# Optimization experiments

Hardware: AMD Instinct MI355X
Metric: run time of the kernel (lower is better)

Reference implementation:

```python
import jax, jax.numpy as jnp
import numpy as np

KERNEL_SIZE = 4  # kernel_size=4, dim=1, degree-1 open B-splines (SplineConv defaults)


def spline_conv(x, edge_index, edge_attr, W, root, bias):
    """SplineConv with dim=1, kernel_size=4, degree=1, open splines, aggr='mean'.

    x: [N, F_in]; edge_index: [2, E] (row 0 = source, row 1 = target);
    edge_attr: [E, 1] pseudo-coords in [0,1]; W: [K, F_in, F_out];
    root: [F_in, F_out]; bias: [F_out].
    """
    N = x.shape[0]
    src, dst = edge_index[0], edge_index[1]
    u = edge_attr[:, 0]                          # [E]
    v = u * (KERNEL_SIZE - 1)                    # open spline: scale by K-1
    vf = jnp.floor(v)
    frac = v - vf                                # [E], degree-1 basis fraction
    k0 = jnp.clip(vf.astype(jnp.int32), 0, KERNEL_SIZE - 1)
    k1 = jnp.minimum(k0 + 1, KERNEL_SIZE - 1)
    # Project node features through all K kernel weights once: [N, K, F_out]
    xw = jnp.einsum('nf,kfo->nko', x, W)
    # Per-edge message: basis-weighted mix of the two active kernel projections
    m = (1.0 - frac)[:, None] * xw[src, k0] + frac[:, None] * xw[src, k1]  # [E, F_out]
    # Mean aggregation at target nodes
    agg = jax.ops.segment_sum(m, dst, num_segments=N)               # [N, F_out]
    deg = jax.ops.segment_sum(jnp.ones_like(u), dst, num_segments=N)
    agg = agg / jnp.maximum(deg, 1.0)[:, None]
    return agg + x @ root + bias


def setup_inputs() -> dict:
    key = jax.random.key(0)
    ks = jax.random.split(key, 9)
    N, E, F_IN, HID, C = 50000, 1600000, 48, 32, 10
    x = jax.random.normal(ks[0], (N, F_IN), dtype=jnp.float32)
    edge_index = jax.random.randint(ks[1], (2, E), 0, N, dtype=jnp.int64)
    edge_attr = jax.random.uniform(ks[2], (E, 1), dtype=jnp.float32)
    s = 0.1
    W1 = jax.random.normal(ks[3], (KERNEL_SIZE, F_IN, HID), dtype=jnp.float32) * s
    root1 = jax.random.normal(ks[4], (F_IN, HID), dtype=jnp.float32) * s
    bias1 = jax.random.normal(ks[5], (HID,), dtype=jnp.float32) * s
    W2 = jax.random.normal(ks[6], (KERNEL_SIZE, HID, C), dtype=jnp.float32) * s
    root2 = jax.random.normal(ks[7], (HID, C), dtype=jnp.float32) * s
    bias2 = jax.random.normal(ks[8], (C,), dtype=jnp.float32) * s
    return {"x": x, "edge_index": edge_index, "edge_attr": edge_attr,
            "W1": W1, "root1": root1, "bias1": bias1,
            "W2": W2, "root2": root2, "bias2": bias2}


def reference(x, edge_index, edge_attr, W1, root1, bias1, W2, root2, bias2):
    # dropout is identity in eval mode (training=self.training)
    h = spline_conv(x, edge_index, edge_attr, W1, root1, bias1)
    h = jax.nn.elu(h)
    h = spline_conv(h, edge_index, edge_attr, W2, root2, bias2)
    return jax.nn.log_softmax(h, axis=1)
```

## Files before the change

### kernel.cpp

```cpp
#include <hip/hip_runtime.h>
#include <math.h>


#define F_IN   48
#define HID    32
#define NCLS   10
#define KS     4
#define BKT_SH 8
#define TILE   4096

__device__ inline unsigned short f2bf(float f) {
    unsigned x = __float_as_uint(f);
    unsigned r = x + 0x7FFFu + ((x >> 16) & 1u);
    return (unsigned short)(r >> 16);
}
__device__ inline float bf2f(unsigned short u) {
    return __uint_as_float(((unsigned)u) << 16);
}


__global__ void bucket_hist_kernel(const int* __restrict__ ei, int* __restrict__ bcnt,
                                   int E, int NB) {
    __shared__ int lcnt[256];
    int t = threadIdx.x;
    lcnt[t] = 0;
    __syncthreads();
    int e0 = blockIdx.x * TILE;
    int n = min(TILE, E - e0);
    for (int r = 0; r < TILE / 256; ++r) {
        int i = r * 256 + t;
        if (i < n) atomicAdd(&lcnt[ei[E + e0 + i] >> BKT_SH], 1);
    }
    __syncthreads();
    if (t < NB && lcnt[t] > 0) atomicAdd(&bcnt[t], lcnt[t]);
}

__global__ void mini_scan_kernel(const int* __restrict__ bcnt, int* __restrict__ bbase,
                                 int* __restrict__ gcur, int NB) {
    __shared__ int a[256], c[256];
    int t = threadIdx.x;
    int v = (t < NB) ? bcnt[t] : 0;
    a[t] = v; c[t] = v;
    __syncthreads();
    for (int o = 1; o < 256; o <<= 1) {
        int w = (t >= o) ? a[t - o] : 0;
        __syncthreads();
        a[t] += w;
        __syncthreads();
    }
    int ex = a[t] - c[t];
    if (t < NB) { bbase[t] = ex; gcur[t] = ex; }
    if (t == 0) bbase[NB] = a[255];
}

__global__ void bucket_scatter_kernel(const int* __restrict__ ei, const float* __restrict__ ea,
                                      int* __restrict__ gcur, uint2* __restrict__ tpd,
                                      int E, int NB) {
    __shared__ unsigned spl[TILE];
    __shared__ unsigned short sdst[TILE];
    __shared__ unsigned short inv[TILE];
    __shared__ int lcnt[256], loff[256], lrank[256], gb[256];
    int t = threadIdx.x;
    lcnt[t] = 0; lrank[t] = 0;
    __syncthreads();
    int e0 = blockIdx.x * TILE;
    int n = min(TILE, E - e0);
    for (int r = 0; r < TILE / 256; ++r) {
        int i = r * 256 + t;
        if (i < n) {
            int e = e0 + i;
            int src = ei[e];
            int dst = ei[E + e];
            float u = ea[e];
            float v = u * (float)(KS - 1);
            float vf = floorf(v);
            int k0 = min(max((int)vf, 0), KS - 1);
            unsigned qf = (unsigned)((v - vf) * 16383.f + 0.5f);
            spl[i] = (unsigned)src | ((unsigned)k0 << 16) | (qf << 18);
            sdst[i] = (unsigned short)dst;
            atomicAdd(&lcnt[dst >> BKT_SH], 1);
        }
    }
    __syncthreads();
    loff[t] = lcnt[t];
    __syncthreads();
    for (int o = 1; o < 256; o <<= 1) {
        int w = (t >= o) ? loff[t - o] : 0;
        __syncthreads();
        loff[t] += w;
        __syncthreads();
    }
    int ex = loff[t] - lcnt[t];
    __syncthreads();
    loff[t] = ex;
    if (t < NB) gb[t] = atomicAdd(&gcur[t], lcnt[t]);
    __syncthreads();
    for (int r = 0; r < TILE / 256; ++r) {
        int i = r * 256 + t;
        if (i < n) {
            int b = sdst[i] >> BKT_SH;
            int p = loff[b] + atomicAdd(&lrank[b], 1);
            inv[p] = (unsigned short)i;
        }
    }
    __syncthreads();
    for (int r = 0; r < TILE / 256; ++r) {
        int j = r * 256 + t;
        if (j < n) {
            int i = inv[j];
            int d = sdst[i];
            int b = d >> BKT_SH;
            int pos = gb[b] + (j - loff[b]);
            tpd[pos] = make_uint2(spl[i], (unsigned)d);
        }
    }
}

__global__ void node_sort_kernel(const uint2* __restrict__ tpd, const int* __restrict__ bbase,
                                 unsigned* __restrict__ spk, int* __restrict__ offs,
                                 int N, int NB) {
    __shared__ int hc[256], hs[256], hr[256];
    int b = blockIdx.x;
    int t = threadIdx.x;
    int nb0 = b << BKT_SH;
    int nb = min(256, N - nb0);
    int base = bbase[b];
    int m = bbase[b + 1] - base;
    hc[t] = 0; hr[t] = 0;
    __syncthreads();
    for (int i = t; i < m; i += 256) atomicAdd(&hc[tpd[base + i].y - nb0], 1);
    __syncthreads();
    hs[t] = hc[t];
    __syncthreads();
    for (int o = 1; o < 256; o <<= 1) {
        int w = (t >= o) ? hs[t - o] : 0;
        __syncthreads();
        hs[t] += w;
        __syncthreads();
    }
    if (t < nb) offs[nb0 + t] = base + (hs[t] - hc[t]);
    if (b == NB - 1 && t == 0) offs[N] = base + m;
    for (int i = t; i < m; i += 256) {
        uint2 rec = tpd[base + i];
        int d = rec.y - nb0;
        int p = (hs[d] - hc[d]) + atomicAdd(&hr[d], 1);
        spk[base + p] = rec.x;
    }
}


__global__ __launch_bounds__(320) void xw1_kernel(
        const float* __restrict__ X, const float* __restrict__ W,
        const float* __restrict__ R, unsigned short* __restrict__ outk,
        float* __restrict__ outr, int n) {
    __shared__ float lw[48 * 160];
    int t = threadIdx.x;
    for (int i = t; i < 48 * 160; i += 320) {
        int f = i / 160;
        int col = i - f * 160;
        lw[i] = (col < 128) ? W[(size_t)(col >> 5) * (48 * 32) + f * 32 + (col & 31)]
                            : R[f * 32 + (col - 128)];
    }
    __syncthreads();
    int g = t % 40;
    int lp = t / 40;
    int n0 = (blockIdx.x * 8 + lp) * 2;
    if (n0 + 1 >= n) return;
    const float4* X0 = (const float4*)(X + (size_t)n0 * F_IN);
    const float4* X1 = (const float4*)(X + (size_t)(n0 + 1) * F_IN);
    float4 x0[12], x1[12];
#pragma unroll
    for (int i = 0; i < 12; ++i) { x0[i] = X0[i]; x1[i] = X1[i]; }
    const float4* lw4 = (const float4*)lw;
    float4 a0 = {0,0,0,0}, a1 = {0,0,0,0};
#pragma unroll
    for (int fb = 0; fb < 12; ++fb) {
        float4 v0 = x0[fb], v1 = x1[fb];
#pragma unroll
        for (int j = 0; j < 4; ++j) {
            float s0 = (j == 0) ? v0.x : (j == 1) ? v0.y : (j == 2) ? v0.z : v0.w;
            float s1 = (j == 0) ? v1.x : (j == 1) ? v1.y : (j == 2) ? v1.z : v1.w;
            float4 w = lw4[(fb * 4 + j) * 40 + g];
            a0.x = fmaf(s0, w.x, a0.x); a0.y = fmaf(s0, w.y, a0.y);
            a0.z = fmaf(s0, w.z, a0.z); a0.w = fmaf(s0, w.w, a0.w);
            a1.x = fmaf(s1, w.x, a1.x); a1.y = fmaf(s1, w.y, a1.y);
            a1.z = fmaf(s1, w.z, a1.z); a1.w = fmaf(s1, w.w, a1.w);
        }
    }
    if (g < 32) {
        uint2 u0, u1;
        u0.x = f2bf(a0.x) | ((unsigned)f2bf(a0.y) << 16);
        u0.y = f2bf(a0.z) | ((unsigned)f2bf(a0.w) << 16);
        u1.x = f2bf(a1.x) | ((unsigned)f2bf(a1.y) << 16);
        u1.y = f2bf(a1.z) | ((unsigned)f2bf(a1.w) << 16);
        *(uint2*)(outk + (size_t)n0 * (KS * HID) + g * 4) = u0;
        *(uint2*)(outk + (size_t)(n0 + 1) * (KS * HID) + g * 4) = u1;
    } else {
        int o = 4 * g - 128;
        *(float4*)(outr + (size_t)n0 * HID + o) = a0;
        *(float4*)(outr + (size_t)(n0 + 1) * HID + o) = a1;
    }
}

__global__ void xw2_kernel(const float* __restrict__ H, const float* __restrict__ W,
                           const float* __restrict__ R, unsigned short* __restrict__ outk,
                           float* __restrict__ outr, int n) {
    __shared__ float lw2[32 * 50];
    int t = threadIdx.x;
    for (int i = t; i < 32 * 50; i += 256) {
        int f = i / 50;
        int col = i - f * 50;
        lw2[i] = (col < 40) ? W[(size_t)(col / 10) * (32 * 10) + f * 10 + (col % 10)]
                            : R[f * 10 + (col - 40)];
    }
    __syncthreads();
    int total = (n / 2) * 25;
    int id = blockIdx.x * blockDim.x + t;
    if (id >= total) return;
    int p = id % 25;
    int pr = id / 25;
    int n0 = 2 * pr;
    const float4* H0 = (const float4*)(H + (size_t)n0 * HID);
    const float4* H1 = (const float4*)(H + (size_t)(n0 + 1) * HID);
    float4 h0[8], h1[8];
#pragma unroll
    for (int i = 0; i < 8; ++i) { h0[i] = H0[i]; h1[i] = H1[i]; }
    const float2* lwp = (const float2*)lw2;
    float ax0 = 0.f, ay0 = 0.f, ax1 = 0.f, ay1 = 0.f;
#pragma unroll
    for (int fb = 0; fb < 8; ++fb) {
        float4 v0 = h0[fb], v1 = h1[fb];
#pragma unroll
        for (int j = 0; j < 4; ++j) {
            float s0 = (j == 0) ? v0.x : (j == 1) ? v0.y : (j == 2) ? v0.z : v0.w;
            float s1 = (j == 0) ? v1.x : (j == 1) ? v1.y : (j == 2) ? v1.z : v1.w;
            float2 w = lwp[(fb * 4 + j) * 25 + p];
            ax0 = fmaf(s0, w.x, ax0); ay0 = fmaf(s0, w.y, ay0);
            ax1 = fmaf(s1, w.x, ax1); ay1 = fmaf(s1, w.y, ay1);
        }
    }
    int col = 2 * p;
    if (col < KS * NCLS) {
        *(unsigned*)(outk + (size_t)n0 * (KS * NCLS) + col) =
            f2bf(ax0) | ((unsigned)f2bf(ay0) << 16);
        *(unsigned*)(outk + (size_t)(n0 + 1) * (KS * NCLS) + col) =
            f2bf(ax1) | ((unsigned)f2bf(ay1) << 16);
    } else {
        int o = col - KS * NCLS;
        *(float2*)(outr + (size_t)n0 * NCLS + o) = make_float2(ax0, ay0);
        *(float2*)(outr + (size_t)(n0 + 1) * NCLS + o) = make_float2(ax1, ay1);
    }
}


#define DECODE32(p, row, dk, fr)                                          \
    {   int src_ = (p) & 0xFFFF;                                          \
        int k0_ = ((p) >> 16) & 3;                                        \
        int k1_ = min(k0_ + 1, KS - 1);                                   \
        fr = (float)((p) >> 18) * (1.f / 16383.f);                        \
        row = xwk + (size_t)src_ * (KS * HID) + k0_ * HID + cg * 4;       \
        dk = (k1_ - k0_) * HID; }

__device__ inline void fma4(uint2 v0, uint2 v1, float fr, float4& a) {
    float w0 = 1.f - fr;
    a.x = fmaf(w0, __uint_as_float(v0.x << 16), a.x);
    a.x = fmaf(fr, __uint_as_float(v1.x << 16), a.x);
    a.y = fmaf(w0, __uint_as_float(v0.x & 0xFFFF0000u), a.y);
    a.y = fmaf(fr, __uint_as_float(v1.x & 0xFFFF0000u), a.y);
    a.z = fmaf(w0, __uint_as_float(v0.y << 16), a.z);
    a.z = fmaf(fr, __uint_as_float(v1.y << 16), a.z);
    a.w = fmaf(w0, __uint_as_float(v0.y & 0xFFFF0000u), a.w);
    a.w = fmaf(fr, __uint_as_float(v1.y & 0xFFFF0000u), a.w);
}

__global__ void agg1_kernel(const unsigned short* __restrict__ xwk,
                            const float* __restrict__ xroot,
                            const int* __restrict__ offs, const unsigned* __restrict__ spk,
                            const float* __restrict__ bias, float* __restrict__ h, int n) {
    int lane = threadIdx.x & 63;
    int cg = lane & 7;
    int slot = lane >> 3;
    int node = blockIdx.x * 4 + (threadIdx.x >> 6);
    if (node >= n) return;
    int beg = offs[node];
    int end = offs[node + 1];
    float4 a0 = {0, 0, 0, 0}, a1 = {0, 0, 0, 0};
    int e = beg + slot;
    while (e + 24 < end) {
        unsigned p0 = spk[e], p1 = spk[e + 8], p2 = spk[e + 16], p3 = spk[e + 24];
        const unsigned short *r0, *r1, *r2, *r3;
        int d0, d1, d2, d3;
        float f0, f1, f2, f3;
        DECODE32(p0, r0, d0, f0);
        DECODE32(p1, r1, d1, f1);
        DECODE32(p2, r2, d2, f2);
        DECODE32(p3, r3, d3, f3);
        uint2 v00 = *(const uint2*)r0, v01 = *(const uint2*)(r0 + d0);
        uint2 v10 = *(const uint2*)r1, v11 = *(const uint2*)(r1 + d1);
        uint2 v20 = *(const uint2*)r2, v21 = *(const uint2*)(r2 + d2);
        uint2 v30 = *(const uint2*)r3, v31 = *(const uint2*)(r3 + d3);
        fma4(v00, v01, f0, a0);
        fma4(v10, v11, f1, a1);
        fma4(v20, v21, f2, a0);
        fma4(v30, v31, f3, a1);
        e += 32;
    }
    while (e < end) {
        unsigned p = spk[e];
        const unsigned short* r;
        int d;
        float f;
        DECODE32(p, r, d, f);
        uint2 v0 = *(const uint2*)r, v1 = *(const uint2*)(r + d);
        fma4(v0, v1, f, a0);
        e += 8;
    }
    float4 s;
    s.x = a0.x + a1.x; s.y = a0.y + a1.y; s.z = a0.z + a1.z; s.w = a0.w + a1.w;
#pragma unroll
    for (int m = 8; m < 64; m <<= 1) {
        s.x += __shfl_xor(s.x, m, 64);
        s.y += __shfl_xor(s.y, m, 64);
        s.z += __shfl_xor(s.z, m, 64);
        s.w += __shfl_xor(s.w, m, 64);
    }
    if (slot == 0) {
        int deg = end - beg;
        float inv = 1.f / (float)(deg > 0 ? deg : 1);
        float4 r = *(const float4*)(xroot + (size_t)node * HID + cg * 4);
        float4 b = *(const float4*)(bias + cg * 4);
        float4 o;
        o.x = fmaf(s.x, inv, r.x + b.x);
        o.y = fmaf(s.y, inv, r.y + b.y);
        o.z = fmaf(s.z, inv, r.z + b.z);
        o.w = fmaf(s.w, inv, r.w + b.w);
        o.x = (o.x > 0.f) ? o.x : expm1f(o.x);
        o.y = (o.y > 0.f) ? o.y : expm1f(o.y);
        o.z = (o.z > 0.f) ? o.z : expm1f(o.z);
        o.w = (o.w > 0.f) ? o.w : expm1f(o.w);
        *(float4*)(h + (size_t)node * HID + cg * 4) = o;
    }
}

__global__ void agg2_kernel(const unsigned short* __restrict__ xwk,
                            const float* __restrict__ xroot,
                            const int* __restrict__ offs, const unsigned* __restrict__ spk,
                            const float* __restrict__ bias, float* __restrict__ out, int n) {
    int lane = threadIdx.x & 63;
    int u = lane & 7;
    int slot = lane >> 3;
    int node = blockIdx.x * 4 + (threadIdx.x >> 6);
    bool nv = node < n;
    if (!nv) node = n - 1;
    int up = min(u, 4);
    int beg = offs[node];
    int end = offs[node + 1];
    float a0l = 0.f, a0h = 0.f, a1l = 0.f, a1h = 0.f;

#define DEC2(p, q0, q1, fr)                                               \
    {   int src_ = (p) & 0xFFFF;                                          \
        int k0_ = ((p) >> 16) & 3;                                        \
        int k1_ = min(k0_ + 1, KS - 1);                                   \
        fr = (float)((p) >> 18) * (1.f / 16383.f);                        \
        const unsigned short* row_ = xwk + (size_t)src_ * 40;             \
        q0 = (const unsigned*)(row_ + k0_ * 10) + up;                     \
        q1 = (const unsigned*)(row_ + k1_ * 10) + up; }

#define FMA2(t0, t1, fr, al, ah)                                          \
    {   float w0_ = 1.f - fr;                                             \
        al = fmaf(w0_, __uint_as_float((t0) << 16), al);                  \
        al = fmaf(fr,  __uint_as_float((t1) << 16), al);                  \
        ah = fmaf(w0_, __uint_as_float((t0) & 0xFFFF0000u), ah);          \
        ah = fmaf(fr,  __uint_as_float((t1) & 0xFFFF0000u), ah); }

    int e = beg + slot;
    while (e + 24 < end) {
        unsigned p0 = spk[e], p1 = spk[e + 8], p2 = spk[e + 16], p3 = spk[e + 24];
        const unsigned *q00, *q01, *q10, *q11, *q20, *q21, *q30, *q31;
        float f0, f1, f2, f3;
        DEC2(p0, q00, q01, f0);
        DEC2(p1, q10, q11, f1);
        DEC2(p2, q20, q21, f2);
        DEC2(p3, q30, q31, f3);
        unsigned t00 = *q00, t01 = *q01;
        unsigned t10 = *q10, t11 = *q11;
        unsigned t20 = *q20, t21 = *q21;
        unsigned t30 = *q30, t31 = *q31;
        FMA2(t00, t01, f0, a0l, a0h);
        FMA2(t10, t11, f1, a1l, a1h);
        FMA2(t20, t21, f2, a0l, a0h);
        FMA2(t30, t31, f3, a1l, a1h);
        e += 32;
    }
    while (e < end) {
        unsigned p = spk[e];
        const unsigned *q0, *q1;
        float f;
        DEC2(p, q0, q1, f);
        unsigned t0 = *q0, t1 = *q1;
        FMA2(t0, t1, f, a0l, a0h);
        e += 8;
    }
    float vl = a0l + a1l, vh = a0h + a1h;
    if (u > 4) { vl = 0.f; vh = 0.f; }
#pragma unroll
    for (int m = 8; m < 64; m <<= 1) {
        vl += __shfl_xor(vl, m, 64);
        vh += __shfl_xor(vh, m, 64);
    }
    int deg = end - beg;
    float invd = 1.f / (float)(deg > 0 ? deg : 1);
    float l0 = -INFINITY, l1 = -INFINITY;
    if (u < 5) {
        float2 xr = *(const float2*)(xroot + (size_t)node * NCLS + 2 * u);
        l0 = fmaf(vl, invd, xr.x + bias[2 * u]);
        l1 = fmaf(vh, invd, xr.y + bias[2 * u + 1]);
    }
    float mx = fmaxf(l0, l1);
#pragma unroll
    for (int m = 1; m < 8; m <<= 1) mx = fmaxf(mx, __shfl_xor(mx, m, 64));
    float sden = (u < 5) ? (expf(l0 - mx) + expf(l1 - mx)) : 0.f;
#pragma unroll
    for (int m = 1; m < 8; m <<= 1) sden += __shfl_xor(sden, m, 64);
    if (nv && slot == 0 && u < 5) {
        float ls = logf(sden);
        *(float2*)(out + (size_t)node * NCLS + 2 * u) =
            make_float2(l0 - mx - ls, l1 - mx - ls);
    }
}

extern "C" void kernel_launch(void* const* d_in, const int* in_sizes, int n_in,
                              void* d_out, int out_size, void* d_ws, size_t ws_size,
                              hipStream_t stream) {
    const float* x       = (const float*)d_in[0];
    const int*   ei      = (const int*)d_in[1];
    const float* ea      = (const float*)d_in[2];
    const float* W1      = (const float*)d_in[3];
    const float* root1   = (const float*)d_in[4];
    const float* bias1   = (const float*)d_in[5];
    const float* W2      = (const float*)d_in[6];
    const float* root2   = (const float*)d_in[7];
    const float* bias2   = (const float*)d_in[8];
    float* out = (float*)d_out;

    const int N = in_sizes[0] / F_IN;
    const int E = in_sizes[2];
    const int NB = (N + 255) >> BKT_SH;

    char* base = (char*)d_ws;
    size_t off = 0;
    auto alloc = [&](size_t bytes) {
        char* p = base + off;
        off = (off + bytes + 255) & ~(size_t)255;
        return (void*)p;
    };
    unsigned short* xwk1 = (unsigned short*)alloc((size_t)N * KS * HID * 2);
    float* xr1           = (float*)alloc((size_t)N * HID * 4);
    float* h             = (float*)alloc((size_t)N * HID * 4);
    int* offs            = (int*)alloc(((size_t)N + 1) * 4);
    int* bcnt            = (int*)alloc((size_t)NB * 4);
    int* bbase           = (int*)alloc(((size_t)NB + 1) * 4);
    int* gcur            = (int*)alloc((size_t)NB * 4);
    unsigned* spk        = (unsigned*)alloc((size_t)E * 4);
    uint2* tpd           = (uint2*)xwk1;
    unsigned short* xwk2 = xwk1;
    float* xr2           = xr1;
    if (ws_size < off) return;

    int ebk = (E + TILE - 1) / TILE;

    hipMemsetAsync(bcnt, 0, (size_t)NB * 4, stream);
    bucket_hist_kernel<<<ebk, 256, 0, stream>>>(ei, bcnt, E, NB);
    mini_scan_kernel<<<1, 256, 0, stream>>>(bcnt, bbase, gcur, NB);
    bucket_scatter_kernel<<<ebk, 256, 0, stream>>>(ei, ea, gcur, tpd, E, NB);
    node_sort_kernel<<<NB, 256, 0, stream>>>(tpd, bbase, spk, offs, N, NB);
    xw1_kernel<<<(N + 15) / 16, 320, 0, stream>>>(x, W1, root1, xwk1, xr1, N);
    agg1_kernel<<<(N + 3) / 4, 256, 0, stream>>>(xwk1, xr1, offs, spk, bias1, h, N);
    {
        int total = (N / 2) * 25;
        xw2_kernel<<<(total + 255) / 256, 256, 0, stream>>>(h, W2, root2, xwk2, xr2, N);
    }
    agg2_kernel<<<(N + 3) / 4, 256, 0, stream>>>(xwk2, xr2, offs, spk, bias2, out, N);
}
```

Before: 247.6 us.

## Fuse node sort and first projection into one launch with block-range dispatch

Merges the per-bucket node sort kernel and the first-layer feature projection into a single kernel. Blocks with index below NB do the sort and the rest do the projection, sharing LDS through a union. Because the two now run concurrently, the edge record buffer gets its own workspace allocation instead of aliasing the projection output. This removes one launch and lets the two independent phases overlap. In exchange it uses 256-thread blocks that only run 240 active projection threads, needs more blocks, and takes extra workspace memory.

```diff
diff --git a/kernel.cpp b/kernel.cpp
--- a/kernel.cpp
+++ b/kernel.cpp
@@ -116,62 +116,65 @@
     }
 }
 
-__global__ void node_sort_kernel(const uint2* __restrict__ tpd, const int* __restrict__ bbase,
-                                 unsigned* __restrict__ spk, int* __restrict__ offs,
-                                 int N, int NB) {
-    __shared__ int hc[256], hs[256], hr[256];
-    int b = blockIdx.x;
-    int t = threadIdx.x;
-    int nb0 = b << BKT_SH;
-    int nb = min(256, N - nb0);
-    int base = bbase[b];
-    int m = bbase[b + 1] - base;
-    hc[t] = 0; hr[t] = 0;
-    __syncthreads();
-    for (int i = t; i < m; i += 256) atomicAdd(&hc[tpd[base + i].y - nb0], 1);
-    __syncthreads();
-    hs[t] = hc[t];
-    __syncthreads();
-    for (int o = 1; o < 256; o <<= 1) {
-        int w = (t >= o) ? hs[t - o] : 0;
-        __syncthreads();
-        hs[t] += w;
-        __syncthreads();
-    }
-    if (t < nb) offs[nb0 + t] = base + (hs[t] - hc[t]);
-    if (b == NB - 1 && t == 0) offs[N] = base + m;
-    for (int i = t; i < m; i += 256) {
-        uint2 rec = tpd[base + i];
-        int d = rec.y - nb0;
-        int p = (hs[d] - hc[d]) + atomicAdd(&hr[d], 1);
-        spk[base + p] = rec.x;
-    }
-}
-
-
-__global__ __launch_bounds__(320) void xw1_kernel(
+
+__global__ __launch_bounds__(256) void nsort_xw1_kernel(
+        const uint2* __restrict__ tpd, const int* __restrict__ bbase,
+        unsigned* __restrict__ spk, int* __restrict__ offs, int N, int NB,
         const float* __restrict__ X, const float* __restrict__ W,
         const float* __restrict__ R, unsigned short* __restrict__ outk,
-        float* __restrict__ outr, int n) {
-    __shared__ float lw[48 * 160];
+        float* __restrict__ outr) {
+    __shared__ union {
+        struct { int hc[256]; int hs[256]; int hr[256]; } ns;
+        float lw[48 * 160];
+    } sm;
     int t = threadIdx.x;
-    for (int i = t; i < 48 * 160; i += 320) {
+    if ((int)blockIdx.x < NB) {
+        int b = blockIdx.x;
+        int nb0 = b << BKT_SH;
+        int nb = min(256, N - nb0);
+        int base = bbase[b];
+        int m = bbase[b + 1] - base;
+        sm.ns.hc[t] = 0; sm.ns.hr[t] = 0;
+        __syncthreads();
+        for (int i = t; i < m; i += 256) atomicAdd(&sm.ns.hc[tpd[base + i].y - nb0], 1);
+        __syncthreads();
+        sm.ns.hs[t] = sm.ns.hc[t];
+        __syncthreads();
+        for (int o = 1; o < 256; o <<= 1) {
+            int w = (t >= o) ? sm.ns.hs[t - o] : 0;
+            __syncthreads();
+            sm.ns.hs[t] += w;
+            __syncthreads();
+        }
+        if (t < nb) offs[nb0 + t] = base + (sm.ns.hs[t] - sm.ns.hc[t]);
+        if (b == NB - 1 && t == 0) offs[N] = base + m;
+        for (int i = t; i < m; i += 256) {
+            uint2 rec = tpd[base + i];
+            int d = rec.y - nb0;
+            int p = (sm.ns.hs[d] - sm.ns.hc[d]) + atomicAdd(&sm.ns.hr[d], 1);
+            spk[base + p] = rec.x;
+        }
+        return;
+    }
+    int bx = blockIdx.x - NB;
+    for (int i = t; i < 48 * 160; i += 256) {
         int f = i / 160;
         int col = i - f * 160;
-        lw[i] = (col < 128) ? W[(size_t)(col >> 5) * (48 * 32) + f * 32 + (col & 31)]
-                            : R[f * 32 + (col - 128)];
+        sm.lw[i] = (col < 128) ? W[(size_t)(col >> 5) * (48 * 32) + f * 32 + (col & 31)]
+                               : R[f * 32 + (col - 128)];
     }
     __syncthreads();
     int g = t % 40;
     int lp = t / 40;
-    int n0 = (blockIdx.x * 8 + lp) * 2;
-    if (n0 + 1 >= n) return;
+    if (lp >= 6) return;
+    int n0 = (bx * 6 + lp) * 2;
+    if (n0 + 1 >= N) return;
     const float4* X0 = (const float4*)(X + (size_t)n0 * F_IN);
     const float4* X1 = (const float4*)(X + (size_t)(n0 + 1) * F_IN);
     float4 x0[12], x1[12];
 #pragma unroll
     for (int i = 0; i < 12; ++i) { x0[i] = X0[i]; x1[i] = X1[i]; }
-    const float4* lw4 = (const float4*)lw;
+    const float4* lw4 = (const float4*)sm.lw;
     float4 a0 = {0,0,0,0}, a1 = {0,0,0,0};
 #pragma unroll
     for (int fb = 0; fb < 12; ++fb) {
@@ -462,19 +465,20 @@
     int* bbase           = (int*)alloc(((size_t)NB + 1) * 4);
     int* gcur            = (int*)alloc((size_t)NB * 4);
     unsigned* spk        = (unsigned*)alloc((size_t)E * 4);
-    uint2* tpd           = (uint2*)xwk1;
+    uint2* tpd           = (uint2*)alloc((size_t)E * 8);
     unsigned short* xwk2 = xwk1;
     float* xr2           = xr1;
     if (ws_size < off) return;
 
     int ebk = (E + TILE - 1) / TILE;
+    int xb  = (N + 11) / 12;
 
     hipMemsetAsync(bcnt, 0, (size_t)NB * 4, stream);
     bucket_hist_kernel<<<ebk, 256, 0, stream>>>(ei, bcnt, E, NB);
     mini_scan_kernel<<<1, 256, 0, stream>>>(bcnt, bbase, gcur, NB);
     bucket_scatter_kernel<<<ebk, 256, 0, stream>>>(ei, ea, gcur, tpd, E, NB);
-    node_sort_kernel<<<NB, 256, 0, stream>>>(tpd, bbase, spk, offs, N, NB);
-    xw1_kernel<<<(N + 15) / 16, 320, 0, stream>>>(x, W1, root1, xwk1, xr1, N);
+    nsort_xw1_kernel<<<NB + xb, 256, 0, stream>>>(tpd, bbase, spk, offs, N, NB,
+                                                  x, W1, root1, xwk1, xr1);
     agg1_kernel<<<(N + 3) / 4, 256, 0, stream>>>(xwk1, xr1, offs, spk, bias1, h, N);
     {
         int total = (N / 2) * 25;
```

Result: faster. 231.7 us, median of 2 (-6.4%).
